# Performance work log

Hardware: AMD Instinct MI355X
Metric: run time of the kernel (lower is better)

The kernel has to match this reference:

```python
import jax, jax.numpy as jnp
import numpy as np

DECAY_MIN = 2.0
DECAY_MAX = 2.0


def setup_inputs() -> dict:
    key = jax.random.key(0)
    k1, k2, k3 = jax.random.split(key, 3)
    x = jax.random.normal(k1, (16, 256, 4096), dtype=jnp.float32)
    kernels = jax.random.normal(k2, (6, 4, 256, 32), dtype=jnp.float32)
    D = jax.random.normal(k3, (4, 256), dtype=jnp.float32)
    return {"x": x, "kernels": kernels, "D": D}


def _build_kernel(kernels):
    # kernels: (num_scales, heads, h, kernel_size)
    num_scales, heads, h, ks = kernels.shape
    multiplier = jnp.linspace(DECAY_MIN, DECAY_MAX, h).reshape(1, -1, 1)  # (1, h, 1)
    parts = []
    for i in range(num_scales):
        rep = 2 ** max(0, i - 1)
        ker = jnp.repeat(kernels[i], rep, axis=-1)  # nearest-neighbor upsample
        parts.append(ker * multiplier ** (num_scales - i - 1))
    k = jnp.concatenate(parts, axis=-1)  # (heads, h, kernel_length)
    # kernel_norm is computed on first forward and detached
    norm = jax.lax.stop_gradient(
        jnp.linalg.norm(k, axis=-1, keepdims=True))
    return k / norm


def reference(x, kernels, D):
    # x: (b, h, L); kernels: (S, heads, h, ks); D: (heads, h)
    b, h, L = x.shape
    heads = kernels.shape[1]
    k = _build_kernel(kernels)                 # (heads, h, KL)
    kernel_length = k.shape[-1]
    n = 2 * L                                  # 'constant' padding mode -> factor 2
    k_f = jnp.fft.rfft(k, n=n)                 # (heads, h, n//2+1)
    u_f = jnp.fft.rfft(x, n=n)                 # (b, h, n//2+1)
    y_f = jnp.einsum('bhl,chl->bchl', u_f, k_f)
    y = jnp.fft.irfft(y_f, n=n)                # (b, heads, h, n)
    s = kernel_length // 2
    y = y[..., s:s + L]                        # (b, heads, h, L)
    # rearrange 'b c h l -> b (h c) l'
    y = jnp.transpose(y, (0, 2, 1, 3)).reshape(b, h * heads, L)
    skip = jnp.einsum('bhl,ch->bchl', x, D)    # (b, heads, h, L)
    skip = jnp.transpose(skip, (0, 2, 1, 3)).reshape(b, h * heads, L)
    return y + skip
```

## Files before the change

### kernel.cpp

```cpp
#include <hip/hip_runtime.h>

#define HEADS 4
#define NH    256
#define LEN   4096
#define NB    16
#define TT    1024
#define NSUB  4

typedef float     f32x4 __attribute__((ext_vector_type(4)));
typedef float     f32x2 __attribute__((ext_vector_type(2)));
typedef _Float16  f16x2 __attribute__((ext_vector_type(2)));
typedef _Float16  f16x8 __attribute__((ext_vector_type(8)));
typedef unsigned  u32x2 __attribute__((ext_vector_type(2)));
typedef unsigned  u32x4 __attribute__((ext_vector_type(4)));

__device__ __forceinline__ unsigned packh(float a, float b) {
    union { _Float16 h[2]; unsigned u; } z;
    z.h[0] = (_Float16)a; z.h[1] = (_Float16)b;
    return z.u;
}
__device__ __forceinline__ unsigned short h16u(float a) {
    union { _Float16 h; unsigned short u; } z;
    z.h = (_Float16)a; return z.u;
}
__device__ __forceinline__ float lo16(unsigned u) {
    return (float)__builtin_bit_cast(f16x2, u)[0];
}
__device__ __forceinline__ float hi16(unsigned u) {
    return (float)__builtin_bit_cast(f16x2, u)[1];
}

__global__ __launch_bounds__(64) void build_wgt_kernel(
    const float* __restrict__ kernels, unsigned short* __restrict__ wtab)
{
    const int h    = blockIdx.x;
    const int lane = threadIdx.x;

    float ssum[4] = {0.f, 0.f, 0.f, 0.f};
    #pragma unroll
    for (int q = 0; q < 3; ++q) {
        const int tap = lane + q * 64;
        const int i = tap >> 5;
        const int j = tap & 31;
        const float scale = (float)(1 << (5 - i));
        const float repf  = (float)(i == 0 ? 1 : (1 << (i - 1)));
        #pragma unroll
        for (int c = 0; c < 4; ++c) {
            const float kv = kernels[(((i * HEADS) + c) * NH + h) * 32 + j];
            const float v  = kv * scale;
            ssum[c] += v * v * repf;
        }
    }
    #pragma unroll
    for (int off = 32; off > 0; off >>= 1) {
        #pragma unroll
        for (int c = 0; c < 4; ++c) ssum[c] += __shfl_xor(ssum[c], off);
    }
    float inv[4];
    #pragma unroll
    for (int c = 0; c < 4; ++c) inv[c] = 1.0f / sqrtf(ssum[c]);

    for (int it = 0; it < 40; ++it) {
        const int idx = it * 64 + lane;
        const int c   = idx / 640;
        const int rem = idx - c * 640;
        const int u   = rem >> 7;
        const int y   = rem & 127;
        const int j   = 95 - y;
        const int J   = (u == 0) ? 64 : 32;
        float val = 0.f;
        if (j >= 0 && j < J) {
            int s, tp;
            if (u == 0) { s = (j < 32) ? 0 : 1; tp = j & 31; }
            else        { s = u + 1;            tp = j;      }
            val = kernels[((s * HEADS + c) * NH + h) * 32 + tp]
                  * (float)(1 << (5 - s)) * inv[c];
        }
        wtab[((h * 4 + c) * 5 + u) * 128 + y] = h16u(val);
    }
}

#define AFB   0
#define HFB   12288
#define ZPB   17408
#define GBASE 17920
#define G1B   (GBASE + 0)
#define G2B   (GBASE + 4160)
#define G4B   (GBASE + 8256)
#define G8B   (GBASE + 12352)
#define G16B  (GBASE + 16448)
#define SMBYTES 38464

#define SWZ(BASE, OFF, SH, MSK) \
    ((char*)SM + (BASE) + ((OFF) ^ ((((OFF) >> (SH)) & (MSK)) << 4)))

#define AFF(CC, FI) \
    (*(const f16x8*)((char*)SM + AFB + ((CC) * 6 + (FI)) * 1024 + lane * 16))
#define AFH(CC, HI) \
    (*(const f16x8*)((char*)SM + hbase + (hmask & (((CC) * 5 + (HI)) * 512))))

#define MFMA16(acc, a, bb) \
    (acc) = __builtin_amdgcn_mfma_f32_16x16x32_f16((a), (bb), (acc), 0, 0, 0)

__global__ __launch_bounds__(256, 4) void conv_kernel(
    const float*           __restrict__ x,
    const unsigned short*  __restrict__ wtab,
    const float*           __restrict__ Dp,
    float*                 __restrict__ out)
{
    __shared__ __align__(16) unsigned char SM[SMBYTES];
    unsigned* DR32 = (unsigned*)(SM + GBASE);

    const int cpair = blockIdx.x;
    const int h     = blockIdx.y;
    const int b     = blockIdx.z;
    const int tid   = threadIdx.x;
    const int w     = tid >> 6;
    const int lane  = tid & 63;
    const int dd    = lane & 15;
    const int qq    = lane >> 4;

    const float* xrow = x + ((size_t)(b * NH + h)) * LEN;

    if (w == 0) {
        #pragma unroll
        for (int cc = 0; cc < 2; ++cc) {
            const int c = cpair * 2 + cc;
            const unsigned short* wpc = wtab + (size_t)((h * 4 + c) * 5) * 128;
            #pragma unroll
            for (int u = 0; u < 5; ++u) {
                const int J  = (u == 0) ? 64 : 32;
                const int nM = (u == 0) ? 3 : 2;
                const unsigned short* wp = wpc + u * 128;
                #pragma unroll
                for (int m = 0; m < 3; ++m) {
                    if (m < nM) {
                        const int y0 = 95 - dd - J + 32 * m + 8 * qq;
                        u32x4 dw;
                        #pragma unroll
                        for (int d = 0; d < 4; ++d)
                            dw[d] = (unsigned)wp[y0 + 2 * d]
                                  | ((unsigned)wp[y0 + 2 * d + 1] << 16);
                        if (m == nM - 1) {
                            if (lane < 32)
                                *(u32x4*)((char*)SM + HFB
                                    + (cc * 5 + u) * 512 + lane * 16) = dw;
                        } else {
                            const int fi = (u == 0) ? m : u + 1;
                            *(u32x4*)((char*)SM + AFB
                                + (cc * 6 + fi) * 1024 + lane * 16) = dw;
                        }
                    }
                }
            }
        }
    }
    if (tid < 32) *(u32x4*)((char*)SM + ZPB + tid * 16) = (u32x4){0, 0, 0, 0};

    const float dC0 = Dp[(cpair * 2 + 0) * NH + h];
    const float dC1 = Dp[(cpair * 2 + 1) * NH + h];

    const int hbase = (lane < 32) ? (HFB + lane * 16) : (ZPB + (lane - 32) * 16);
    const int hmask = (lane < 32) ? ~0 : 0;

    const int kap = 16 * w + dd;
    const int E0B = 32 * kap + 1920 + 16 * qq;
    const int E1B = 2048 * (kap & 1)  + 32 * (kap >> 1) + 896 + 16 * qq;
    const int E2B = 1024 * (kap & 3)  + 32 * (kap >> 2) + 384 + 16 * qq;
    const int E3B = 512  * (kap & 7)  + 32 * (kap >> 3) + 128 + 16 * qq;
    const int E4B = 256  * (kap & 15) + 32 * (kap >> 4)       + 16 * qq;

    for (int st = 0; st < NSUB; ++st) {
        const int t0s = st * TT;
        __syncthreads();

        {
            const int bg = t0s - 544 + 8 * tid;
            float v[40];
            #pragma unroll
            for (int blk = 0; blk < 10; ++blk) {
                const int g = bg + 4 * blk;
                f32x4 t;
                if (g >= 0 && g + 3 < LEN) {
                    t = *(const f32x4*)(xrow + g);
                } else {
                    #pragma unroll
                    for (int e = 0; e < 4; ++e) {
                        const int gg = g + e;
                        t[e] = (gg >= 0 && gg < LEN) ? xrow[gg] : 0.f;
                    }
                }
                v[4 * blk] = t.x; v[4 * blk + 1] = t.y;
                v[4 * blk + 2] = t.z; v[4 * blk + 3] = t.w;
            }
            {
                u32x4 px;
                px[0] = packh(v[32], v[33]); px[1] = packh(v[34], v[35]);
                px[2] = packh(v[36], v[37]); px[3] = packh(v[38], v[39]);
                *(u32x4*)SWZ(G1B, 16 * tid, 7, 1) = px;
            }
            if (tid < 4)
                *(u32x4*)SWZ(G1B, 4096 + 16 * tid, 7, 1) = (u32x4){0, 0, 0, 0};

            #pragma unroll
            for (int j = 39; j >= 2; --j) v[j] += v[j - 1];
            #pragma unroll
            for (int ph = 0; ph < 2; ++ph) {
                u32x2 pw;
                pw.x = packh(v[32 + ph], v[34 + ph]);
                pw.y = packh(v[36 + ph], v[38 + ph]);
                *(u32x2*)SWZ(G2B, 2048 * ph + 8 * tid, 7, 1) = pw;
            }
            #pragma unroll
            for (int j = 39; j >= 4; --j) v[j] += v[j - 2];
            #pragma unroll
            for (int ph = 0; ph < 4; ++ph)
                *(unsigned*)SWZ(G4B, 1024 * ph + 4 * tid, 10, 1) =
                    packh(v[32 + ph], v[36 + ph]);
            #pragma unroll
            for (int j = 39; j >= 8; --j) v[j] += v[j - 4];
            #pragma unroll
            for (int e = 0; e < 8; ++e)
                *(unsigned short*)SWZ(G8B, 512 * e + 2 * tid, 9, 7) =
                    h16u(v[32 + e]);
            #pragma unroll
            for (int j = 39; j >= 16; --j) v[j] += v[j - 8];
            #pragma unroll
            for (int e = 0; e < 8; ++e) {
                const int E = 8 * (tid & 1) + e;
                *(unsigned short*)SWZ(G16B, 256 * E + 2 * (tid >> 1), 8, 7) =
                    h16u(v[32 + e]);
            }
        }
        __syncthreads();

        f32x4 DA[2][5];
        #pragma unroll
        for (int cc = 0; cc < 2; ++cc)
            #pragma unroll
            for (int u = 0; u < 5; ++u) DA[cc][u] = (f32x4){0.f, 0.f, 0.f, 0.f};

        {
            const f16x8 b0 = *(const f16x8*)SWZ(G1B, E0B,       7, 1);
            const f16x8 b1 = *(const f16x8*)SWZ(G1B, E0B + 64,  7, 1);
            const f16x8 b2 = *(const f16x8*)SWZ(G1B, E0B + 128, 7, 1);
            #pragma unroll
            for (int cc = 0; cc < 2; ++cc) {
                MFMA16(DA[cc][0], AFF(cc, 0), b0);
                MFMA16(DA[cc][0], AFF(cc, 1), b1);
                MFMA16(DA[cc][0], AFH(cc, 0), b2);
            }
        }
        {
            const f16x8 b0 = *(const f16x8*)SWZ(G2B, E1B,      7, 1);
            const f16x8 b1 = *(const f16x8*)SWZ(G2B, E1B + 64, 7, 1);
            #pragma unroll
            for (int cc = 0; cc < 2; ++cc) {
                MFMA16(DA[cc][1], AFF(cc, 2), b0);
                MFMA16(DA[cc][1], AFH(cc, 1), b1);
            }
        }
        {
            const f16x8 b0 = *(const f16x8*)SWZ(G4B, E2B,      10, 1);
            const f16x8 b1 = *(const f16x8*)SWZ(G4B, E2B + 64, 10, 1);
            #pragma unroll
            for (int cc = 0; cc < 2; ++cc) {
                MFMA16(DA[cc][2], AFF(cc, 3), b0);
                MFMA16(DA[cc][2], AFH(cc, 2), b1);
            }
        }
        {
            const f16x8 b0 = *(const f16x8*)SWZ(G8B, E3B,      9, 7);
            const f16x8 b1 = *(const f16x8*)SWZ(G8B, E3B + 64, 9, 7);
            #pragma unroll
            for (int cc = 0; cc < 2; ++cc) {
                MFMA16(DA[cc][3], AFF(cc, 4), b0);
                MFMA16(DA[cc][3], AFH(cc, 3), b1);
            }
        }
        {
            const f16x8 b0 = *(const f16x8*)SWZ(G16B, E4B,      8, 7);
            const f16x8 b1 = *(const f16x8*)SWZ(G16B, E4B + 64, 8, 7);
            #pragma unroll
            for (int cc = 0; cc < 2; ++cc) {
                MFMA16(DA[cc][4], AFF(cc, 5), b0);
                MFMA16(DA[cc][4], AFH(cc, 4), b1);
            }
        }
        __syncthreads();

        f32x4 a0 = (f32x4){0.f, 0.f, 0.f, 0.f};
        f32x4 a1 = (f32x4){0.f, 0.f, 0.f, 0.f};

#define DRWRITE(U) do {                                                   \
        const int row_ = w * 64 + lane;                                   \
        _Pragma("unroll")                                                 \
        for (int e = 0; e < 4; ++e)                                       \
            DR32[row_ * 5 + e] = packh(DA[0][U][e], DA[1][U][e]);         \
    } while (0)

        {
            DRWRITE(0);
            const int sL = (lane >> 2) + 16 * (lane & 3);
            const int rb = (w * 64 + sL) * 5;
            #pragma unroll
            for (int e = 0; e < 4; ++e) {
                const unsigned q = DR32[rb + e];
                a0[e] += lo16(q); a1[e] += hi16(q);
            }
        }
        {
            DRWRITE(1);
            const int da = (2 * lane) & 15;
            const int uu = lane >> 3;
            const int L  = 2 * uu + 16 * (da >> 2);
            const int bi = (w * 64 + L) * 5 + (da & 3);
            const unsigned qa = DR32[bi],     qb = DR32[bi + 1];
            const unsigned qc = DR32[bi + 5], qd = DR32[bi + 6];
            a0[0] += lo16(qa); a1[0] += hi16(qa);
            a0[2] += lo16(qb); a1[2] += hi16(qb);
            a0[1] += lo16(qc); a1[1] += hi16(qc);
            a0[3] += lo16(qd); a1[3] += hi16(qd);
        }
        {
            DRWRITE(2);
            const int de = lane & 15;
            const int uu = lane >> 4;
            const int L0 = 4 * uu + 16 * (de >> 2);
            const int rb = w * 64 + L0;
            #pragma unroll
            for (int e = 0; e < 4; ++e) {
                const unsigned q = DR32[(rb + e) * 5 + (de & 3)];
                a0[e] += lo16(q); a1[e] += hi16(q);
            }
        }
        {
            DRWRITE(3);
            const int de = (lane >> 1) & 15;
            const int uu = lane >> 5;
            const int L0 = 8 * uu + 4 * (lane & 1) + 16 * (de >> 2);
            const int rb = w * 64 + L0;
            #pragma unroll
            for (int e = 0; e < 4; ++e) {
                const unsigned q = DR32[(rb + e) * 5 + (de & 3)];
                a0[e] += lo16(q); a1[e] += hi16(q);
            }
        }
        {
            DRWRITE(4);
            const int de = (lane >> 2) & 15;
            const int L0 = 4 * (lane & 3) + 16 * (de >> 2);
            const int rb = w * 64 + L0;
            #pragma unroll
            for (int e = 0; e < 4; ++e) {
                const unsigned q = DR32[(rb + e) * 5 + (de & 3)];
                a0[e] += lo16(q); a1[e] += hi16(q);
            }
        }
#undef DRWRITE

        const int gt = t0s + 256 * w + 4 * lane;
        const f32x4 xv = *(const f32x4*)(xrow + gt);
        const size_t ob = ((size_t)(b * NH + h) * 4 + cpair * 2) * LEN + gt;
        *(f32x4*)(out + ob)       = a0 + xv * dC0;
        *(f32x4*)(out + ob + LEN) = a1 + xv * dC1;
    }
}

extern "C" void kernel_launch(void* const* d_in, const int* in_sizes, int n_in,
                              void* d_out, int out_size, void* d_ws, size_t ws_size,
                              hipStream_t stream)
{
    const float* x       = (const float*)d_in[0];
    const float* kernels = (const float*)d_in[1];
    const float* D       = (const float*)d_in[2];
    float*       out     = (float*)d_out;
    unsigned short* wtab = (unsigned short*)d_ws;

    build_wgt_kernel<<<256, 64, 0, stream>>>(kernels, wtab);
    conv_kernel<<<dim3(2, NH, NB), 256, 0, stream>>>(x, wtab, D, out);
}
```

Measured before the change: 165.4 us.

## Swap MFMA operands to cut LDS transposes and merge scale accumulators

Scale 4 is now accumulated into the same MFMA accumulator as scale 0, and scales 1-3 use swapped A/B operands so their outputs land in a transposed layout. That removes five per-scale LDS write/read transposes in favour of one packed vector write per scale and three vector reads, using a per-wave LDS region. The aim is to cut LDS traffic and instruction count in the epilogue. The remaining transposes still round-trip through fp16, and the new index mapping must match the output layout exactly.

```diff
diff --git a/kernel.cpp b/kernel.cpp
--- a/kernel.cpp
+++ b/kernel.cpp
@@ -8,7 +8,6 @@
 #define NSUB  4
 
 typedef float     f32x4 __attribute__((ext_vector_type(4)));
-typedef float     f32x2 __attribute__((ext_vector_type(2)));
 typedef _Float16  f16x2 __attribute__((ext_vector_type(2)));
 typedef _Float16  f16x8 __attribute__((ext_vector_type(8)));
 typedef unsigned  u32x2 __attribute__((ext_vector_type(2)));
@@ -109,7 +108,6 @@
     float*                 __restrict__ out)
 {
     __shared__ __align__(16) unsigned char SM[SMBYTES];
-    unsigned* DR32 = (unsigned*)(SM + GBASE);
 
     const int cpair = blockIdx.x;
     const int h     = blockIdx.y;
@@ -119,6 +117,8 @@
     const int lane  = tid & 63;
     const int dd    = lane & 15;
     const int qq    = lane >> 4;
+
+    unsigned* DRW = (unsigned*)(SM + GBASE + w * 3072);
 
     const float* xrow = x + ((size_t)(b * NH + h)) * LEN;
 
@@ -170,6 +170,11 @@
     const int E3B = 512  * (kap & 7)  + 32 * (kap >> 3) + 128 + 16 * qq;
     const int E4B = 256  * (kap & 15) + 32 * (kap >> 4)       + 16 * qq;
 
+    const int wB = 64 * qq + 4 * dd;
+    const int wC = 128 * (qq >> 1) + 8 * dd + 4 * (qq & 1);
+    const int wD = 64 * qq + 2 * dd;
+    const int rA = 16 * dd + 4 * qq;
+
     for (int st = 0; st < NSUB; ++st) {
         const int t0s = st * TT;
         __syncthreads();
@@ -234,11 +239,14 @@
         }
         __syncthreads();
 
-        f32x4 DA[2][5];
-        #pragma unroll
-        for (int cc = 0; cc < 2; ++cc)
-            #pragma unroll
-            for (int u = 0; u < 5; ++u) DA[cc][u] = (f32x4){0.f, 0.f, 0.f, 0.f};
+        f32x4 DA_A[2], DA_B[2], DA_C[2], DA_D[2];
+        #pragma unroll
+        for (int cc = 0; cc < 2; ++cc) {
+            DA_A[cc] = (f32x4){0.f, 0.f, 0.f, 0.f};
+            DA_B[cc] = (f32x4){0.f, 0.f, 0.f, 0.f};
+            DA_C[cc] = (f32x4){0.f, 0.f, 0.f, 0.f};
+            DA_D[cc] = (f32x4){0.f, 0.f, 0.f, 0.f};
+        }
 
         {
             const f16x8 b0 = *(const f16x8*)SWZ(G1B, E0B,       7, 1);
@@ -246,9 +254,9 @@
             const f16x8 b2 = *(const f16x8*)SWZ(G1B, E0B + 128, 7, 1);
             #pragma unroll
             for (int cc = 0; cc < 2; ++cc) {
-                MFMA16(DA[cc][0], AFF(cc, 0), b0);
-                MFMA16(DA[cc][0], AFF(cc, 1), b1);
-                MFMA16(DA[cc][0], AFH(cc, 0), b2);
+                MFMA16(DA_A[cc], AFF(cc, 0), b0);
+                MFMA16(DA_A[cc], AFF(cc, 1), b1);
+                MFMA16(DA_A[cc], AFH(cc, 0), b2);
             }
         }
         {
@@ -256,8 +264,8 @@
             const f16x8 b1 = *(const f16x8*)SWZ(G2B, E1B + 64, 7, 1);
             #pragma unroll
             for (int cc = 0; cc < 2; ++cc) {
-                MFMA16(DA[cc][1], AFF(cc, 2), b0);
-                MFMA16(DA[cc][1], AFH(cc, 1), b1);
+                MFMA16(DA_D[cc], b0, AFF(cc, 2));
+                MFMA16(DA_D[cc], b1, AFH(cc, 1));
             }
         }
         {
@@ -265,8 +273,8 @@
             const f16x8 b1 = *(const f16x8*)SWZ(G4B, E2B + 64, 10, 1);
             #pragma unroll
             for (int cc = 0; cc < 2; ++cc) {
-                MFMA16(DA[cc][2], AFF(cc, 3), b0);
-                MFMA16(DA[cc][2], AFH(cc, 2), b1);
+                MFMA16(DA_B[cc], b0, AFF(cc, 3));
+                MFMA16(DA_B[cc], b1, AFH(cc, 2));
             }
         }
         {
@@ -274,8 +282,8 @@
             const f16x8 b1 = *(const f16x8*)SWZ(G8B, E3B + 64, 9, 7);
             #pragma unroll
             for (int cc = 0; cc < 2; ++cc) {
-                MFMA16(DA[cc][3], AFF(cc, 4), b0);
-                MFMA16(DA[cc][3], AFH(cc, 3), b1);
+                MFMA16(DA_C[cc], b0, AFF(cc, 4));
+                MFMA16(DA_C[cc], b1, AFH(cc, 3));
             }
         }
         {
@@ -283,85 +291,43 @@
             const f16x8 b1 = *(const f16x8*)SWZ(G16B, E4B + 64, 8, 7);
             #pragma unroll
             for (int cc = 0; cc < 2; ++cc) {
-                MFMA16(DA[cc][4], AFF(cc, 5), b0);
-                MFMA16(DA[cc][4], AFH(cc, 4), b1);
+                MFMA16(DA_A[cc], b0, AFF(cc, 5));
+                MFMA16(DA_A[cc], b1, AFH(cc, 4));
             }
         }
         __syncthreads();
 
-        f32x4 a0 = (f32x4){0.f, 0.f, 0.f, 0.f};
-        f32x4 a1 = (f32x4){0.f, 0.f, 0.f, 0.f};
-
-#define DRWRITE(U) do {                                                   \
-        const int row_ = w * 64 + lane;                                   \
-        _Pragma("unroll")                                                 \
-        for (int e = 0; e < 4; ++e)                                       \
-            DR32[row_ * 5 + e] = packh(DA[0][U][e], DA[1][U][e]);         \
-    } while (0)
-
-        {
-            DRWRITE(0);
-            const int sL = (lane >> 2) + 16 * (lane & 3);
-            const int rb = (w * 64 + sL) * 5;
+        {
+            u32x4 pB, pC;
+            u32x2 pD0, pD1;
             #pragma unroll
             for (int e = 0; e < 4; ++e) {
-                const unsigned q = DR32[rb + e];
-                a0[e] += lo16(q); a1[e] += hi16(q);
-            }
-        }
-        {
-            DRWRITE(1);
-            const int da = (2 * lane) & 15;
-            const int uu = lane >> 3;
-            const int L  = 2 * uu + 16 * (da >> 2);
-            const int bi = (w * 64 + L) * 5 + (da & 3);
-            const unsigned qa = DR32[bi],     qb = DR32[bi + 1];
-            const unsigned qc = DR32[bi + 5], qd = DR32[bi + 6];
-            a0[0] += lo16(qa); a1[0] += hi16(qa);
-            a0[2] += lo16(qb); a1[2] += hi16(qb);
-            a0[1] += lo16(qc); a1[1] += hi16(qc);
-            a0[3] += lo16(qd); a1[3] += hi16(qd);
-        }
-        {
-            DRWRITE(2);
-            const int de = lane & 15;
-            const int uu = lane >> 4;
-            const int L0 = 4 * uu + 16 * (de >> 2);
-            const int rb = w * 64 + L0;
-            #pragma unroll
-            for (int e = 0; e < 4; ++e) {
-                const unsigned q = DR32[(rb + e) * 5 + (de & 3)];
-                a0[e] += lo16(q); a1[e] += hi16(q);
-            }
-        }
-        {
-            DRWRITE(3);
-            const int de = (lane >> 1) & 15;
-            const int uu = lane >> 5;
-            const int L0 = 8 * uu + 4 * (lane & 1) + 16 * (de >> 2);
-            const int rb = w * 64 + L0;
-            #pragma unroll
-            for (int e = 0; e < 4; ++e) {
-                const unsigned q = DR32[(rb + e) * 5 + (de & 3)];
-                a0[e] += lo16(q); a1[e] += hi16(q);
-            }
-        }
-        {
-            DRWRITE(4);
-            const int de = (lane >> 2) & 15;
-            const int L0 = 4 * (lane & 3) + 16 * (de >> 2);
-            const int rb = w * 64 + L0;
-            #pragma unroll
-            for (int e = 0; e < 4; ++e) {
-                const unsigned q = DR32[(rb + e) * 5 + (de & 3)];
-                a0[e] += lo16(q); a1[e] += hi16(q);
-            }
-        }
-#undef DRWRITE
-
-        const int gt = t0s + 256 * w + 4 * lane;
+                pB[e] = packh(DA_B[0][e], DA_B[1][e]);
+                pC[e] = packh(DA_C[0][e], DA_C[1][e]);
+            }
+            pD0.x = packh(DA_D[0][0], DA_D[1][0]);
+            pD0.y = packh(DA_D[0][1], DA_D[1][1]);
+            pD1.x = packh(DA_D[0][2], DA_D[1][2]);
+            pD1.y = packh(DA_D[0][3], DA_D[1][3]);
+            *(u32x4*)&DRW[wB]            = pB;
+            *(u32x4*)&DRW[256 + wC]      = pC;
+            *(u32x2*)&DRW[512 + wD]      = pD0;
+            *(u32x2*)&DRW[512 + wD + 32] = pD1;
+        }
+        const u32x4 qB = *(const u32x4*)&DRW[rA];
+        const u32x4 qC = *(const u32x4*)&DRW[256 + rA];
+        const u32x4 qD = *(const u32x4*)&DRW[512 + rA];
+
+        const int gt = t0s + 256 * w + rA;
         const f32x4 xv = *(const f32x4*)(xrow + gt);
         const size_t ob = ((size_t)(b * NH + h) * 4 + cpair * 2) * LEN + gt;
+
+        f32x4 a0, a1;
+        #pragma unroll
+        for (int e = 0; e < 4; ++e) {
+            a0[e] = DA_A[0][e] + lo16(qB[e]) + lo16(qC[e]) + lo16(qD[e]);
+            a1[e] = DA_A[1][e] + hi16(qB[e]) + hi16(qC[e]) + hi16(qD[e]);
+        }
         *(f32x4*)(out + ob)       = a0 + xv * dC0;
         *(f32x4*)(out + ob + LEN) = a1 + xv * dC1;
     }
```

Measured after the change: 148.3 us. -10.3%, faster.
